# Optimization experiments

Hardware: AMD Instinct MI355X
Metric: run time of the kernel (lower is better)

Reference implementation:

```python
import jax, jax.numpy as jnp
import numpy as np

KS = 7            # kernel_size
DIL = 1           # dilatation
H = 96
W = 96
PAD = DIL * (KS - 1) // 2
SHIFTS = [s * DIL for s in range(KS)]


def stack_kernel(a, axis=-2):
    # a: [B, H+2*PAD, W+2*PAD, C] -> [B, H, W, ks^2, C] (or stacked on `axis`)
    return jnp.stack([a[:, y:H + y, x:W + x] for y in SHIFTS for x in SHIFTS], axis=axis)


def make_padding_mask():
    # zeros inside, -inf in the halo; stacked per window position -> [1,H,W,ks^2]
    z = jnp.pad(jnp.zeros((1, H, W, 1), jnp.float32),
                ((0, 0), (PAD, PAD), (PAD, PAD), (0, 0)),
                constant_values=-jnp.inf)
    return stack_kernel(z, axis=-1)[..., 0, :]  # [1,H,W,ks^2]


def setup_inputs() -> dict:
    key = jax.random.key(0)
    ks = jax.random.split(key, 8)
    B, C, KD, OD = 2, 128, 64, 128
    Q = jax.random.normal(ks[0], (B, H, W, C), jnp.float32)
    K = jax.random.normal(ks[1], (B, H, W, C), jnp.float32)
    V = jax.random.normal(ks[2], (B, H, W, C), jnp.float32)
    s = 1.0 / np.sqrt(C)
    Wq = jax.random.normal(ks[3], (C, KD), jnp.float32) * s
    Wk = jax.random.normal(ks[4], (C, KD), jnp.float32) * s
    Wv = jax.random.normal(ks[5], (C, OD), jnp.float32) * s
    return {"Q": Q, "K": K, "V": V,
            "Wq": Wq, "bq": jnp.zeros((KD,), jnp.float32),
            "Wk": Wk, "bk": jnp.zeros((KD,), jnp.float32),
            "Wv": Wv, "bv": jnp.zeros((OD,), jnp.float32)}


def reference(Q, K, V, Wq, bq, Wk, bk, Wv, bv):
    # Dense projections (key_dim is not None)
    q = Q @ Wq + bq                      # [B,H,W,KD]
    k = K @ Wk + bk                      # [B,H,W,KD]
    Dk = jnp.asarray(q.shape[-1], q.dtype)

    pad4 = ((0, 0), (PAD, PAD), (PAD, PAD), (0, 0))
    k_stk = stack_kernel(jnp.pad(k, pad4), axis=-2)   # [B,H,W,ks^2,KD]
    mask = make_padding_mask()                        # [1,H,W,ks^2]

    # w = Q . K_neighbors + padding mask; softmax over ks^2 window
    w = jnp.einsum('bhwd,bhwkd->bhwk', q, k_stk) + mask
    scores = jax.nn.softmax(w / jnp.sqrt(Dk), axis=-1)  # [B,H,W,ks^2]

    v_stk = stack_kernel(jnp.pad(V, pad4), axis=-2)   # [B,H,W,ks^2,E]
    out = jnp.einsum('bhwk,bhwke->bhwe', scores, v_stk)
    # V_d Dense with relu (out_dim is not None)
    out = jax.nn.relu(out @ Wv + bv)                  # [B,H,W,out_dim]
    return out
```

## Files before the change

kernel.cpp:

```cpp
#include <hip/hip_runtime.h>
#include <math.h>

#define BH 2
#define HH 96
#define WW 96
#define NPIX (BH*HH*WW)

#define TH 8
#define TW 4
#define NH 140

#define NEGBIG (-3.0e38f)

typedef __attribute__((ext_vector_type(8))) short short8;
typedef __attribute__((ext_vector_type(4))) float f32x4;

__device__ __forceinline__ unsigned short f2bf(float f) {
    union { float f; unsigned u; } a; a.f = f;
    return (unsigned short)((a.u + 0x7FFFu + ((a.u >> 16) & 1u)) >> 16);
}
__device__ __forceinline__ unsigned packbf(float lo, float hi) {
    return (unsigned)f2bf(lo) | ((unsigned)f2bf(hi) << 16);
}

#define WT_STRIDE 136

__global__ __launch_bounds__(256) void prep_proj_kernel(
    const float* __restrict__ Qg, const float* __restrict__ Kg,
    const float* __restrict__ Wq, const float* __restrict__ bq,
    const float* __restrict__ Wk, const float* __restrict__ bk,
    const float* __restrict__ Wv,
    unsigned short* __restrict__ q_bf, unsigned short* __restrict__ k_bf,
    unsigned short* __restrict__ WvT)
{
    __shared__ unsigned short WT[64 * WT_STRIDE];
    const int bid = blockIdx.x;
    const int tid = threadIdx.x;

    if (bid < 576) {
        const bool isq = bid < 288;
        const float* __restrict__ X   = isq ? Qg : Kg;
        const float* __restrict__ Wt  = isq ? Wq : Wk;
        const float* __restrict__ bia = isq ? bq : bk;
        unsigned short* __restrict__ Y = isq ? q_bf : k_bf;

        {
            const float4* __restrict__ W4 = reinterpret_cast<const float4*>(Wt);
            #pragma unroll
            for (int i = 0; i < 8; ++i) {
                const int e  = tid + 256 * i;
                const int k  = e >> 4;
                const int n4 = (e & 15) * 4;
                const float4 v = W4[e];
                WT[(n4 + 0) * WT_STRIDE + k] = f2bf(v.x);
                WT[(n4 + 1) * WT_STRIDE + k] = f2bf(v.y);
                WT[(n4 + 2) * WT_STRIDE + k] = f2bf(v.z);
                WT[(n4 + 3) * WT_STRIDE + k] = f2bf(v.w);
            }
        }
        __syncthreads();

        const int lane = tid & 63;
        const int wvv  = tid >> 6;
        const int row0 = ((bid % 288) * 4 + wvv) * 16;
        const int qd = lane >> 4, m = lane & 15;

        short8 afr[4];
        #pragma unroll
        for (int ks = 0; ks < 4; ++ks) {
            const float4* __restrict__ src = reinterpret_cast<const float4*>(
                X + (size_t)(row0 + m) * 128 + ks * 32 + qd * 8);
            const float4 a0 = src[0], a1 = src[1];
            short8 f;
            f[0] = (short)f2bf(a0.x); f[1] = (short)f2bf(a0.y);
            f[2] = (short)f2bf(a0.z); f[3] = (short)f2bf(a0.w);
            f[4] = (short)f2bf(a1.x); f[5] = (short)f2bf(a1.y);
            f[6] = (short)f2bf(a1.z); f[7] = (short)f2bf(a1.w);
            afr[ks] = f;
        }

        #pragma unroll
        for (int n = 0; n < 4; ++n) {
            f32x4 acc = {};
            #pragma unroll
            for (int ks = 0; ks < 4; ++ks) {
                const short8 bfr = *reinterpret_cast<const short8*>(
                    &WT[(n * 16 + m) * WT_STRIDE + ks * 32 + qd * 8]);
                acc = __builtin_amdgcn_mfma_f32_16x16x32_bf16(afr[ks], bfr, acc, 0, 0, 0);
            }
            const int col = n * 16 + m;
            const float bb = bia[col];
            #pragma unroll
            for (int r = 0; r < 4; ++r)
                Y[(size_t)(row0 + qd * 4 + r) * 64 + col] = f2bf(acc[r] + bb);
        }
    } else {
        const int base = (bid - 576) * 1024 + tid * 4;
        #pragma unroll
        for (int i = 0; i < 4; ++i) {
            const int e = base + i;
            WvT[e] = f2bf(Wv[(e & 127) * 128 + (e >> 7)]);
        }
    }
}

#define PS_OFF 0
#define PS_STRIDE 168
#define AS_OFF 5376
#define AS_STRIDE 136
#define SM_OFF 9728
#define V_OFF 10240
#define VS 160
#define LDS_N 30720

__global__ __launch_bounds__(512) void attn_kernel(
    const unsigned short* __restrict__ q_bf, const unsigned short* __restrict__ k_bf,
    const float* __restrict__ V, const unsigned short* __restrict__ WvT,
    const float* __restrict__ bv, float* __restrict__ out)
{
    __shared__ unsigned short lds[LDS_N];
    const int tid  = threadIdx.x;
    const int lane = tid & 63;
    const int wv   = tid >> 6;
    const int mt   = wv & 1;
    const int ng   = wv >> 1;

    const int bid  = blockIdx.x;
    const int bimg = bid / 288;
    const int tidx = bid % 288;
    const int ty = tidx / 24, tx = tidx % 24;
    const int y0 = ty * TH, x0 = tx * TW;

    const int qd = lane >> 4, m = lane & 15;

    float* __restrict__ smf = reinterpret_cast<float*>(&lds[SM_OFF]);

    {
        const int q4  = tid & 31;
        const int pp0 = tid >> 5;
        const int fsw = (q4 >> 1) & 7;
        unsigned* __restrict__ vl32 = reinterpret_cast<unsigned*>(&lds[V_OFF]);
        #pragma unroll
        for (int rnd = 0; rnd < 5; ++rnd) {
            const int pp  = rnd * 16 + pp0;
            const int p0p = pp * 2;
            int o0, o1;
            {
                const int hy = (p0p * 6554) >> 16;
                const int hx = p0p - hy * 10;
                const int iy = y0 - 3 + hy, ix = x0 - 3 + hx;
                const bool ok = ((unsigned)iy < HH) & ((unsigned)ix < WW) & (p0p < NH);
                o0 = ok ? ((bimg * HH + iy) * WW + ix) : 0;
            }
            {
                const int p1p = p0p + 1;
                const int hy = (p1p * 6554) >> 16;
                const int hx = p1p - hy * 10;
                const int iy = y0 - 3 + hy, ix = x0 - 3 + hx;
                const bool ok = ((unsigned)iy < HH) & ((unsigned)ix < WW) & (p1p < NH);
                o1 = ok ? ((bimg * HH + iy) * WW + ix) : 0;
            }
            const float4 a = *reinterpret_cast<const float4*>(V + (size_t)o0 * 128 + q4 * 4);
            const float4 b = *reinterpret_cast<const float4*>(V + (size_t)o1 * 128 + q4 * 4);
            const int pb   = rnd * 4 + (pp0 >> 2);
            const int sb   = pb ^ ((pb < 16) ? fsw : (fsw & 3));
            const int colw = sb * 4 + (pp & 3);
            const int rb   = q4 * 4;
            vl32[(rb + 0) * (VS / 2) + colw] = packbf(a.x, b.x);
            vl32[(rb + 1) * (VS / 2) + colw] = packbf(a.y, b.y);
            vl32[(rb + 2) * (VS / 2) + colw] = packbf(a.z, b.z);
            vl32[(rb + 3) * (VS / 2) + colw] = packbf(a.w, b.w);
        }
    }

    short8 qa[2];
    {
        const int py = mt * 4 + (m >> 2), px = m & 3;
        const size_t gq = (size_t)(bimg * HH + y0 + py) * WW + (x0 + px);
        #pragma unroll
        for (int ks = 0; ks < 2; ++ks)
            qa[ks] = *reinterpret_cast<const short8*>(q_bf + gq * 64 + ks * 32 + qd * 8);
    }

    const int ntbase = (ng < 2) ? ng * 3 : 6 + (ng - 2) * 2;
    const int ntcnt  = (ng < 2) ? 3 : 2;

    f32x4 sc[3];
    #pragma unroll
    for (int n5 = 0; n5 < 3; ++n5) {
        if (n5 >= ntcnt) break;
        const int h  = (ntbase + n5) * 16 + m;
        const int hy = (h * 6554) >> 16;
        const int hx = h - hy * 10;
        const int iy = y0 - 3 + hy, ix = x0 - 3 + hx;
        const bool ok = ((unsigned)iy < HH) & ((unsigned)ix < WW) & (h < NH);
        const size_t ob = ok ? (size_t)((bimg * HH + iy) * WW + ix) * 64 : 0;
        f32x4 a = {};
        #pragma unroll
        for (int ks = 0; ks < 2; ++ks) {
            const short8 bfr = *reinterpret_cast<const short8*>(k_bf + ob + ks * 32 + qd * 8);
            a = __builtin_amdgcn_mfma_f32_16x16x32_bf16(qa[ks], bfr, a, 0, 0, 0);
        }
        sc[n5] = a;
    }

    float mx[4] = {NEGBIG, NEGBIG, NEGBIG, NEGBIG};
    #pragma unroll
    for (int n5 = 0; n5 < 3; ++n5) {
        if (n5 >= ntcnt) break;
        const int h  = (ntbase + n5) * 16 + m;
        const int hy = (h * 6554) >> 16;
        const int hx = h - hy * 10;
        const int iy = y0 - 3 + hy, ix = x0 - 3 + hx;
        const bool imgok = ((unsigned)iy < HH) & ((unsigned)ix < WW) & (h < NH);
        const int py = mt * 4 + qd;
        #pragma unroll
        for (int r = 0; r < 4; ++r) {
            const bool ok = imgok & ((unsigned)(hy - py) <= 6u) & ((unsigned)(hx - r) <= 6u);
            const float s = ok ? sc[n5][r] * 0.125f : NEGBIG;
            sc[n5][r] = s;
            mx[r] = fmaxf(mx[r], s);
        }
    }
    #pragma unroll
    for (int r = 0; r < 4; ++r)
        #pragma unroll
        for (int off = 1; off < 16; off <<= 1)
            mx[r] = fmaxf(mx[r], __shfl_xor(mx[r], off));

    float sm[4] = {0.f, 0.f, 0.f, 0.f};
    #pragma unroll
    for (int n5 = 0; n5 < 3; ++n5) {
        if (n5 >= ntcnt) break;
        #pragma unroll
        for (int r = 0; r < 4; ++r) {
            const float s = sc[n5][r];
            const float e = (s > -1.0e38f) ? __expf(s - mx[r]) : 0.f;
            sc[n5][r] = e;
            sm[r] += e;
        }
    }
    #pragma unroll
    for (int r = 0; r < 4; ++r)
        #pragma unroll
        for (int off = 1; off < 16; off <<= 1)
            sm[r] += __shfl_xor(sm[r], off);

    if (m == 0) {
        #pragma unroll
        for (int r = 0; r < 4; ++r) {
            const int row = mt * 16 + qd * 4 + r;
            smf[row * 4 + ng]       = mx[r];
            smf[128 + row * 4 + ng] = sm[r];
        }
    }
    __syncthreads();

    float fac[4];
    #pragma unroll
    for (int r = 0; r < 4; ++r) {
        const int row = mt * 16 + qd * 4 + r;
        float M = smf[row * 4 + 0];
        M = fmaxf(M, smf[row * 4 + 1]);
        M = fmaxf(M, smf[row * 4 + 2]);
        M = fmaxf(M, smf[row * 4 + 3]);
        float S = 0.f;
        #pragma unroll
        for (int g = 0; g < 4; ++g) {
            const float mg = smf[row * 4 + g];
            const float eg = (mg > -1.0e38f) ? __expf(mg - M) : 0.f;
            S += smf[128 + row * 4 + g] * eg;
        }
        const float eo = (mx[r] > -1.0e38f) ? __expf(mx[r] - M) : 0.f;
        fac[r] = eo / S;
    }

    #pragma unroll
    for (int n5 = 0; n5 < 3; ++n5) {
        if (n5 >= ntcnt) break;
        #pragma unroll
        for (int r = 0; r < 4; ++r) {
            const int row = mt * 16 + qd * 4 + r;
            const int col = (ntbase + n5) * 16 + m;
            lds[PS_OFF + row * PS_STRIDE + col] = f2bf(sc[n5][r] * fac[r]);
        }
    }
    __syncthreads();

    short8 pa[5];
    #pragma unroll
    for (int ks = 0; ks < 5; ++ks)
        pa[ks] = *reinterpret_cast<const short8*>(
            &lds[PS_OFF + (mt * 16 + m) * PS_STRIDE + ks * 32 + qd * 8]);

    f32x4 oacc[2] = {};
    #pragma unroll
    for (int ks = 0; ks < 5; ++ks) {
        const int kb = ks * 4 + qd;
        #pragma unroll
        for (int n2 = 0; n2 < 2; ++n2) {
            const int ch = (ng * 2 + n2) * 16 + m;
            const int f  = (ch >> 3) & 7;
            const int sb = kb ^ ((kb < 16) ? f : (f & 3));
            const short8 bfr = *reinterpret_cast<const short8*>(
                &lds[V_OFF + ch * VS + sb * 8]);
            oacc[n2] = __builtin_amdgcn_mfma_f32_16x16x32_bf16(pa[ks], bfr, oacc[n2], 0, 0, 0);
        }
    }

    #pragma unroll
    for (int n2 = 0; n2 < 2; ++n2)
        #pragma unroll
        for (int r = 0; r < 4; ++r) {
            const int row = mt * 16 + qd * 4 + r;
            const int col = (ng * 2 + n2) * 16 + m;
            lds[AS_OFF + row * AS_STRIDE + col] = f2bf(oacc[n2][r]);
        }
    __syncthreads();

    short8 aa[4];
    #pragma unroll
    for (int ks = 0; ks < 4; ++ks)
        aa[ks] = *reinterpret_cast<const short8*>(
            &lds[AS_OFF + (mt * 16 + m) * AS_STRIDE + ks * 32 + qd * 8]);

    #pragma unroll
    for (int n2 = 0; n2 < 2; ++n2) {
        const int nt = ng * 2 + n2;
        f32x4 a = {};
        #pragma unroll
        for (int ks = 0; ks < 4; ++ks) {
            const short8 bfr = *reinterpret_cast<const short8*>(
                WvT + (nt * 16 + m) * 128 + ks * 32 + qd * 8);
            a = __builtin_amdgcn_mfma_f32_16x16x32_bf16(aa[ks], bfr, a, 0, 0, 0);
        }
        const int col = nt * 16 + m;
        const float bb = bv[col];
        #pragma unroll
        for (int r = 0; r < 4; ++r) {
            const int py = mt * 4 + qd, px = r;
            const size_t gp = (size_t)(bimg * HH + y0 + py) * WW + (x0 + px);
            out[gp * 128 + col] = fmaxf(a[r] + bb, 0.f);
        }
    }
}

extern "C" void kernel_launch(void* const* d_in, const int* in_sizes, int n_in,
                              void* d_out, int out_size, void* d_ws, size_t ws_size,
                              hipStream_t stream)
{
    const float* Q  = (const float*)d_in[0];
    const float* K  = (const float*)d_in[1];
    const float* V  = (const float*)d_in[2];
    const float* Wq = (const float*)d_in[3];
    const float* bq = (const float*)d_in[4];
    const float* Wk = (const float*)d_in[5];
    const float* bk = (const float*)d_in[6];
    const float* Wv = (const float*)d_in[7];
    const float* bv = (const float*)d_in[8];
    float* out = (float*)d_out;

    unsigned short* wbase = (unsigned short*)d_ws;
    unsigned short* WvT   = wbase + 16384;
    unsigned short* q_bf  = wbase + 32768;
    unsigned short* k_bf  = q_bf + (size_t)NPIX * 64;

    prep_proj_kernel<<<592, 256, 0, stream>>>(Q, K, Wq, bq, Wk, bk, Wv,
                                              q_bf, k_bf, WvT);
    attn_kernel<<<576, 512, 0, stream>>>(q_bf, k_bf, V, WvT, bv, out);
}
```

Measured before the change: 110.6 us.

## Drop softmax max pass, defer normalization to PV output, prefetch Wv fragments

```diff
diff --git a/kernel.cpp b/kernel.cpp
--- a/kernel.cpp
+++ b/kernel.cpp
@@ -113,7 +113,7 @@
 #define VS 160
 #define LDS_N 30720
 
-__global__ __launch_bounds__(512) void attn_kernel(
+__global__ __launch_bounds__(512, 4) void attn_kernel(
     const unsigned short* __restrict__ q_bf, const unsigned short* __restrict__ k_bf,
     const float* __restrict__ V, const unsigned short* __restrict__ WvT,
     const float* __restrict__ bv, float* __restrict__ out)
@@ -204,7 +204,7 @@
         sc[n5] = a;
     }
 
-    float mx[4] = {NEGBIG, NEGBIG, NEGBIG, NEGBIG};
+    float sm[4] = {0.f, 0.f, 0.f, 0.f};
     #pragma unroll
     for (int n5 = 0; n5 < 3; ++n5) {
         if (n5 >= ntcnt) break;
@@ -214,30 +214,14 @@
         const int iy = y0 - 3 + hy, ix = x0 - 3 + hx;
         const bool imgok = ((unsigned)iy < HH) & ((unsigned)ix < WW) & (h < NH);
         const int py = mt * 4 + qd;
+        const int col = (ntbase + n5) * 16 + m;
         #pragma unroll
         for (int r = 0; r < 4; ++r) {
             const bool ok = imgok & ((unsigned)(hy - py) <= 6u) & ((unsigned)(hx - r) <= 6u);
-            const float s = ok ? sc[n5][r] * 0.125f : NEGBIG;
-            sc[n5][r] = s;
-            mx[r] = fmaxf(mx[r], s);
-        }
-    }
-    #pragma unroll
-    for (int r = 0; r < 4; ++r)
-        #pragma unroll
-        for (int off = 1; off < 16; off <<= 1)
-            mx[r] = fmaxf(mx[r], __shfl_xor(mx[r], off));
-
-    float sm[4] = {0.f, 0.f, 0.f, 0.f};
-    #pragma unroll
-    for (int n5 = 0; n5 < 3; ++n5) {
-        if (n5 >= ntcnt) break;
-        #pragma unroll
-        for (int r = 0; r < 4; ++r) {
-            const float s = sc[n5][r];
-            const float e = (s > -1.0e38f) ? __expf(s - mx[r]) : 0.f;
-            sc[n5][r] = e;
+            const float e = ok ? __expf(sc[n5][r] * 0.125f) : 0.f;
             sm[r] += e;
+            const int row = mt * 16 + qd * 4 + r;
+            lds[PS_OFF + row * PS_STRIDE + col] = f2bf(e);
         }
     }
     #pragma unroll
@@ -250,8 +234,7 @@
         #pragma unroll
         for (int r = 0; r < 4; ++r) {
             const int row = mt * 16 + qd * 4 + r;
-            smf[row * 4 + ng]       = mx[r];
-            smf[128 + row * 4 + ng] = sm[r];
+            smf[row * 4 + ng] = sm[r];
         }
     }
     __syncthreads();
@@ -260,32 +243,18 @@
     #pragma unroll
     for (int r = 0; r < 4; ++r) {
         const int row = mt * 16 + qd * 4 + r;
-        float M = smf[row * 4 + 0];
-        M = fmaxf(M, smf[row * 4 + 1]);
-        M = fmaxf(M, smf[row * 4 + 2]);
-        M = fmaxf(M, smf[row * 4 + 3]);
-        float S = 0.f;
-        #pragma unroll
-        for (int g = 0; g < 4; ++g) {
-            const float mg = smf[row * 4 + g];
-            const float eg = (mg > -1.0e38f) ? __expf(mg - M) : 0.f;
-            S += smf[128 + row * 4 + g] * eg;
-        }
-        const float eo = (mx[r] > -1.0e38f) ? __expf(mx[r] - M) : 0.f;
-        fac[r] = eo / S;
-    }
-
-    #pragma unroll
-    for (int n5 = 0; n5 < 3; ++n5) {
-        if (n5 >= ntcnt) break;
-        #pragma unroll
-        for (int r = 0; r < 4; ++r) {
-            const int row = mt * 16 + qd * 4 + r;
-            const int col = (ntbase + n5) * 16 + m;
-            lds[PS_OFF + row * PS_STRIDE + col] = f2bf(sc[n5][r] * fac[r]);
-        }
-    }
-    __syncthreads();
+        const float S = smf[row * 4 + 0] + smf[row * 4 + 1]
+                      + smf[row * 4 + 2] + smf[row * 4 + 3];
+        fac[r] = 1.0f / S;
+    }
+
+    short8 wf[2][4];
+    #pragma unroll
+    for (int n2 = 0; n2 < 2; ++n2)
+        #pragma unroll
+        for (int ks = 0; ks < 4; ++ks)
+            wf[n2][ks] = *reinterpret_cast<const short8*>(
+                WvT + ((ng * 2 + n2) * 16 + m) * 128 + ks * 32 + qd * 8);
 
     short8 pa[5];
     #pragma unroll
@@ -314,7 +283,7 @@
         for (int r = 0; r < 4; ++r) {
             const int row = mt * 16 + qd * 4 + r;
             const int col = (ng * 2 + n2) * 16 + m;
-            lds[AS_OFF + row * AS_STRIDE + col] = f2bf(oacc[n2][r]);
+            lds[AS_OFF + row * AS_STRIDE + col] = f2bf(oacc[n2][r] * fac[r]);
         }
     __syncthreads();
 
@@ -329,11 +298,8 @@
         const int nt = ng * 2 + n2;
         f32x4 a = {};
         #pragma unroll
-        for (int ks = 0; ks < 4; ++ks) {
-            const short8 bfr = *reinterpret_cast<const short8*>(
-                WvT + (nt * 16 + m) * 128 + ks * 32 + qd * 8);
-            a = __builtin_amdgcn_mfma_f32_16x16x32_bf16(aa[ks], bfr, a, 0, 0, 0);
-        }
+        for (int ks = 0; ks < 4; ++ks)
+            a = __builtin_amdgcn_mfma_f32_16x16x32_bf16(aa[ks], wf[n2][ks], a, 0, 0, 0);
         const int col = nt * 16 + m;
         const float bb = bv[col];
         #pragma unroll
@@ -354,8 +320,8 @@
     const float* V  = (const float*)d_in[2];
     const float* Wq = (const float*)d_in[3];
     const float* bq = (const float*)d_in[4];
+    const float* bk = (const float*)d_in[6];
     const float* Wk = (const float*)d_in[5];
-    const float* bk = (const float*)d_in[6];
     const float* Wv = (const float*)d_in[7];
     const float* bv = (const float*)d_in[8];
     float* out = (float*)d_out;
```

Result: no change. 109.5 us (-1.0%).
